# Kernel tuning notes

Hardware: AMD Instinct MI355X
Metric: run time of the kernel (lower is better)

The kernel has to match this reference:

```python
import jax, jax.numpy as jnp
import numpy as np

B, SMAX, TMAX, D = 8, 4096, 4096, 528


def setup_inputs() -> dict:
    key = jax.random.key(0)
    ks = jax.random.split(key, 20)
    src_lens = (np.arange(B) * 256 + 2048).astype(np.int64)  # 2048..3840, sum 23552
    tgt_lens = (np.arange(B) * 224 + 2304).astype(np.int64)  # 2304..3872, sum 24704
    Ns, Nt = int(src_lens.sum()), int(tgt_lens.sum())
    N = Ns + Nt  # 48256 packed coarse points (src then tgt)
    src_mask = jnp.asarray(np.arange(SMAX)[None, :] < src_lens[:, None])
    tgt_mask = jnp.asarray(np.arange(TMAX)[None, :] < tgt_lens[:, None])
    sics = np.concatenate([b * SMAX + np.arange(l) for b, l in enumerate(src_lens)])
    tics = np.concatenate([b * TMAX + np.arange(l) for b, l in enumerate(tgt_lens)])
    w = lambda k, shape: (jax.random.normal(k, shape, jnp.float32) * 0.02)
    return dict(
        geo_feats=jax.random.normal(ks[0], (N, D), jnp.float32),
        pcd=jax.random.normal(ks[1], (N, 3), jnp.float32),
        Wi1=w(ks[2], (528, 528)), bi1=w(ks[3], (528,)),
        Wi2=w(ks[4], (1024, 528)), bi2=w(ks[5], (1024,)),
        Wc1=w(ks[6], (528, 528)), bc1=w(ks[7], (528,)),
        Wc2=w(ks[8], (1024, 528)), bc2=w(ks[9], (1024,)),
        Ws1=w(ks[10], (512, 2576)), bs1=w(ks[11], (512,)),
        Ws2=w(ks[12], (256, 512)), bs2=w(ks[13], (256,)),
        Ws3=w(ks[14], (1, 256)), bs3=w(ks[15], (1,)),
        src_mask=src_mask, tgt_mask=tgt_mask,
        src_ind_coarse_split=jnp.asarray(sics, jnp.int32),
        tgt_ind_coarse_split=jnp.asarray(tics, jnp.int32),
        src_ind_coarse=jnp.arange(Ns, dtype=jnp.int32),
        tgt_ind_coarse=Ns + jnp.arange(Nt, dtype=jnp.int32),
    )


def _scatter(vals, flat_idx, b, n, d):
    # split_feats: zeros[b*n, d]; out[flat_idx] = vals; view(b, n, d)
    return jnp.zeros((b * n, d), vals.dtype).at[flat_idx].set(vals).reshape(b, n, d)


def _pw(x, W, b):
    # pointwise Conv1d(in->out, k=1) as a batched matmul over positions
    return jnp.einsum('bnd,od->bno', x, W) + b


def reference(geo_feats, pcd, Wi1, bi1, Wi2, bi2, Wc1, bc1, Wc2, bc2,
              Ws1, bs1, Ws2, bs2, Ws3, bs3,
              src_mask, tgt_mask, src_ind_coarse_split, tgt_ind_coarse_split,
              src_ind_coarse, tgt_ind_coarse):
    b, smax = src_mask.shape
    tmax = tgt_mask.shape[1]
    d = geo_feats.shape[-1]

    # split_feats: ragged gather -> padded [B, pts_max, D]
    src_feats = _scatter(geo_feats[src_ind_coarse], src_ind_coarse_split, b, smax, d)
    tgt_feats = _scatter(geo_feats[tgt_ind_coarse], tgt_ind_coarse_split, b, tmax, d)
    s_pcd = _scatter(pcd[src_ind_coarse], src_ind_coarse_split, b, smax, 3)
    t_pcd = _scatter(pcd[tgt_ind_coarse], tgt_ind_coarse_split, b, tmax, 3)

    sm = src_mask.astype(src_feats.dtype)
    tm = tgt_mask.astype(tgt_feats.dtype)

    # inst_global over valid src points (per-sample slice -> masked mean)
    h = jax.nn.relu(_pw(src_feats, Wi1, bi1))
    h = jax.nn.relu(_pw(h, Wi2, bi2))                      # [B, Smax, 1024]
    inst_g = jnp.einsum('bno,bn->bo', h, sm) / sm.sum(1, keepdims=True)

    # category_global over valid tgt points
    g = jax.nn.relu(_pw(tgt_feats, Wc1, bc1))
    g = jax.nn.relu(_pw(g, Wc2, bc2))                      # [B, Tmax, 1024]
    cat_g = jnp.einsum('bno,bn->bo', g, tm) / tm.sum(1, keepdims=True)

    # scale_net on concat(src_feats, inst_g, cat_g) without materializing [B,N,2576]:
    # split first conv weight over the concat axis; globals contribute per-batch constants
    Ws1_s, Ws1_i, Ws1_c = Ws1[:, :d], Ws1[:, d:d + 1024], Ws1[:, d + 1024:]
    glob = inst_g @ Ws1_i.T + cat_g @ Ws1_c.T + bs1        # [B, 512]
    z = jax.nn.relu(jnp.einsum('bnd,od->bno', src_feats, Ws1_s) + glob[:, None, :])
    z = jax.nn.relu(_pw(z, Ws2, bs2))                      # [B, Smax, 256]
    s = _pw(z, Ws3, bs3)                                   # [B, Smax, 1]
    scale_mat = jax.nn.sigmoid(s).transpose(0, 2, 1) - 0.5  # [B, 1, Smax]

    inv = 1.0 / jnp.sqrt(jnp.asarray(d, src_feats.dtype))
    return (src_feats * inv, tgt_feats * inv, s_pcd, t_pcd, scale_mat)
```

## Files before the change

### kernel.cpp

```cpp
#include <hip/hip_runtime.h>
#include <hip/hip_bf16.h>
#include <cstdint>
#include <cstddef>

typedef float f32x4 __attribute__((ext_vector_type(4)));
typedef __bf16 bf16x8v __attribute__((ext_vector_type(8)));

#define BM 128
#define BN 128
#define BK 32

__device__ __forceinline__ void gld16(const void* g, void* l) {
  __builtin_amdgcn_global_load_lds((const __attribute__((address_space(1))) void*)g,
                                   (__attribute__((address_space(3))) void*)l, 16, 0, 0);
}


__global__ void build_maps_kernel(const int* __restrict__ sics, int Ns,
                                  const int* __restrict__ tics, int Nt,
                                  int* __restrict__ cnt) {
  int j = blockIdx.x * 256 + threadIdx.x;
  if (j < Ns) {
    if (j == 0) { cnt[0] = 0; cnt[8] = Ns; }
    else { int b = sics[j] >> 12; if ((sics[j - 1] >> 12) != b) cnt[b] = j; }
  }
  if (j < Nt) {
    if (j == 0) { cnt[9] = 0; cnt[17] = Nt; }
    else { int b = tics[j] >> 12; if ((tics[j - 1] >> 12) != b) cnt[9 + b] = j; }
  }
}

struct PrepParams {
  const float* src[6];
  __hip_bfloat16* dst[6];
  int sld[6], rows[6], K[6], Kpad[6], rows_pad[6];
  float* zbuf; int ztotal;
};

__global__ void prep_kernel(PrepParams P) {
  int job = blockIdx.y;
  int i = blockIdx.x * 256 + threadIdx.x;
  if (job == 6) {
    if (i < P.ztotal) P.zbuf[i] = 0.f;
    return;
  }
  int kp = P.Kpad[job];
  int total = P.rows_pad[job] * kp;
  if (i >= total) return;
  int r = i / kp;
  int k = i - r * kp;
  float v = (r < P.rows[job] && k < P.K[job]) ? P.src[job][(size_t)r * P.sld[job] + k] : 0.f;
  P.dst[job][i] = __float2bfloat16(v);
}

template<int EPI>
__global__ __launch_bounds__(256, 2)
void gemm_kernel(const __hip_bfloat16* __restrict__ Aptr, int lda,
                 const __hip_bfloat16* __restrict__ Bw, int ldb,
                 const float* __restrict__ bias,
                 float* __restrict__ red_acc,
                 const float* __restrict__ globv,
                 const int* __restrict__ ridx,
                 __hip_bfloat16* __restrict__ outp, int ldo,
                 int M, int N, int Kpad, int storepad)
{
  __shared__ alignas(16) __hip_bfloat16 lA[BM * BK];
  __shared__ alignas(16) __hip_bfloat16 lB[BN * BK];
  const int tid  = threadIdx.x;
  const int lane = tid & 63;
  const int wave = tid >> 6;
  const int quad = lane >> 4;
  const int l16  = lane & 15;
  const int wr   = wave >> 1;
  const int wc   = wave & 1;
  const int m0   = blockIdx.x * BM;
  const int n0   = blockIdx.y * BN;

  const int srow = tid >> 2;
  const int skel = (tid & 3) << 3;
  const __hip_bfloat16* a0 = Aptr + (size_t)(m0 + srow) * lda + skel;
  const __hip_bfloat16* a1 = Aptr + (size_t)(m0 + 64 + srow) * lda + skel;
  const __hip_bfloat16* b0 = Bw + (size_t)(n0 + srow) * ldb + skel;
  const __hip_bfloat16* b1 = Bw + (size_t)(n0 + 64 + srow) * ldb + skel;
  __hip_bfloat16* lA0 = &lA[tid * 8];
  __hip_bfloat16* lA1 = &lA[2048 + tid * 8];
  __hip_bfloat16* lB0 = &lB[tid * 8];
  __hip_bfloat16* lB1 = &lB[2048 + tid * 8];

  f32x4 acc[4][4];
  const f32x4 zero4 = {0.f, 0.f, 0.f, 0.f};
#pragma unroll
  for (int i = 0; i < 4; ++i)
#pragma unroll
    for (int j = 0; j < 4; ++j) acc[i][j] = zero4;

  for (int k0 = 0; k0 < Kpad; k0 += BK) {
    gld16(a0 + k0, lA0);
    gld16(a1 + k0, lA1);
    gld16(b0 + k0, lB0);
    gld16(b1 + k0, lB1);
    __syncthreads();
    bf16x8v af[4], bfr[4];
#pragma unroll
    for (int i = 0; i < 4; ++i) {
      af[i]  = *(const bf16x8v*)&lA[(wr * 64 + i * 16 + l16) * BK + quad * 8];
      bfr[i] = *(const bf16x8v*)&lB[(wc * 64 + i * 16 + l16) * BK + quad * 8];
    }
#pragma unroll
    for (int mi = 0; mi < 4; ++mi)
#pragma unroll
      for (int ni = 0; ni < 4; ++ni)
        acc[mi][ni] = __builtin_amdgcn_mfma_f32_16x16x32_bf16(af[mi], bfr[ni], acc[mi][ni], 0, 0, 0);
    __syncthreads();
  }

  if (EPI == 1) {
    const int b0r = ridx[m0] >> 12;
#pragma unroll
    for (int ni = 0; ni < 4; ++ni) {
      const int col = n0 + wc * 64 + ni * 16 + l16;
      const bool colok = col < N;
      const float bcol = colok ? bias[col] : 0.f;
#pragma unroll
      for (int mi = 0; mi < 4; ++mi) {
        float v0 = 0.f, v1 = 0.f;
#pragma unroll
        for (int r = 0; r < 4; ++r) {
          const int row = m0 + wr * 64 + mi * 16 + quad * 4 + r;
          const float v = fmaxf(acc[mi][ni][r] + bcol, 0.f);
          const int b = ridx[row] >> 12;
          if (b == b0r) v0 += v; else v1 += v;
        }
        v0 += __shfl_xor(v0, 16, 64); v0 += __shfl_xor(v0, 32, 64);
        v1 += __shfl_xor(v1, 16, 64); v1 += __shfl_xor(v1, 32, 64);
        if (quad == 0 && colok) {
          atomicAdd(&red_acc[b0r * N + col], v0);
          if (b0r + 1 < 8 && v1 != 0.f) atomicAdd(&red_acc[(b0r + 1) * N + col], v1);
        }
      }
    }
  } else {
#pragma unroll
    for (int mi = 0; mi < 4; ++mi) {
#pragma unroll
      for (int r = 0; r < 4; ++r) {
        const int row = m0 + wr * 64 + mi * 16 + quad * 4 + r;
        int b = 0;
        if (EPI == 2) b = ridx[row] >> 12;
#pragma unroll
        for (int ni = 0; ni < 4; ++ni) {
          const int col = n0 + wc * 64 + ni * 16 + l16;
          if (col < N) {
            float v = acc[mi][ni][r];
            v += (EPI == 2) ? globv[b * N + col] : bias[col];
            v = fmaxf(v, 0.f);
            outp[(size_t)row * ldo + col] = __float2bfloat16(v);
          } else if (col < storepad) {
            outp[(size_t)row * ldo + col] = __float2bfloat16(0.f);
          }
        }
      }
    }
  }
}

__global__ __launch_bounds__(256) void glob_kernel(const float* __restrict__ iacc,
                                                   const float* __restrict__ cacc,
                                                   const int* __restrict__ cnt,
                                                   const float* __restrict__ Ws1,
                                                   const float* __restrict__ bs1,
                                                   float* __restrict__ globv) {
  int w    = (blockIdx.x * 256 + threadIdx.x) >> 6;
  int lane = threadIdx.x & 63;
  int b = w >> 9;
  int o = w & 511;
  const float* wi  = Ws1 + (size_t)o * 2576 + 528;
  const float* wcp = Ws1 + (size_t)o * 2576 + 1552;
  float a1 = 0.f, a2 = 0.f;
  for (int k = lane; k < 1024; k += 64) {
    a1 += iacc[b * 1024 + k] * wi[k];
    a2 += cacc[b * 1024 + k] * wcp[k];
  }
  for (int off = 32; off; off >>= 1) {
    a1 += __shfl_xor(a1, off, 64);
    a2 += __shfl_xor(a2, off, 64);
  }
  if (lane == 0) {
    float ns = (float)(cnt[b + 1] - cnt[b]);
    float nt = (float)(cnt[9 + b + 1] - cnt[9 + b]);
    globv[b * 512 + o] = bs1[o] + a1 / ns + a2 / nt;
  }
}

__global__ __launch_bounds__(256) void s_empty_kernel(const float* __restrict__ globv,
                                                      const float* __restrict__ Ws2,
                                                      const float* __restrict__ bs2,
                                                      const float* __restrict__ Ws3,
                                                      const float* __restrict__ bs3,
                                                      float* __restrict__ semp) {
  __shared__ float zrow[512];
  __shared__ float wsum[4];
  int b = blockIdx.x, t = threadIdx.x;
  zrow[t]       = fmaxf(globv[b * 512 + t], 0.f);
  zrow[t + 256] = fmaxf(globv[b * 512 + t + 256], 0.f);
  __syncthreads();
  float acc = bs2[t];
  for (int o = 0; o < 512; ++o) acc += zrow[o] * Ws2[t * 512 + o];
  float p = fmaxf(acc, 0.f) * Ws3[t];
  for (int off = 32; off; off >>= 1) p += __shfl_xor(p, off, 64);
  if ((t & 63) == 0) wsum[t >> 6] = p;
  __syncthreads();
  if (t == 0) semp[b] = wsum[0] + wsum[1] + wsum[2] + wsum[3] + bs3[0];
}

__global__ __launch_bounds__(256) void s_dot_kernel(const __hip_bfloat16* __restrict__ z2,
                                                    const float* __restrict__ Ws3,
                                                    const float* __restrict__ bs3,
                                                    float* __restrict__ sbuf, int M) {
  int w = (blockIdx.x * 256 + threadIdx.x) >> 6;
  int lane = threadIdx.x & 63;
  if (w >= M) return;
  const __hip_bfloat16* zr = z2 + (size_t)w * 256;
  float a = 0.f;
  for (int k = lane; k < 256; k += 64) a += __bfloat162float(zr[k]) * Ws3[k];
  for (int off = 32; off; off >>= 1) a += __shfl_xor(a, off, 64);
  if (lane == 0) sbuf[w] = a + bs3[0];
}

__global__ __launch_bounds__(128)
void fill_feats_kernel(const float* __restrict__ geo, const float* __restrict__ pcd,
                       const int* __restrict__ cnt,
                       float* __restrict__ out0, float* __restrict__ out1,
                       float* __restrict__ out2, float* __restrict__ out3,
                       __hip_bfloat16* __restrict__ geo_b, int Ns, float inv) {
  int bid = blockIdx.x;
  bool is_t = bid >= 32768;
  int pos = is_t ? bid - 32768 : bid;
  int b = pos >> 12, r = pos & 4095;
  int base = is_t ? cnt[9 + b] : cnt[b];
  int lim  = (is_t ? cnt[9 + b + 1] : cnt[b + 1]) - base;
  int t = threadIdx.x;
  float* op = (is_t ? out1 : out0) + (size_t)pos * 528;
  float* pp = (is_t ? out3 : out2) + (size_t)pos * 3;
  if (r < lim) {
    int src_row = (is_t ? Ns : 0) + base + r;
    const float4* g = (const float4*)(geo + (size_t)src_row * 528);
    ushort4* gb = (ushort4*)(geo_b + (size_t)src_row * 544);
    for (int d = t; d < 136; d += 128) {
      if (d < 132) {
        float4 v = g[d];
        float4 s; s.x = v.x * inv; s.y = v.y * inv; s.z = v.z * inv; s.w = v.w * inv;
        ((float4*)op)[d] = s;
        __hip_bfloat16 h0 = __float2bfloat16(v.x), h1 = __float2bfloat16(v.y);
        __hip_bfloat16 h2 = __float2bfloat16(v.z), h3 = __float2bfloat16(v.w);
        ushort4 u;
        u.x = *(unsigned short*)&h0; u.y = *(unsigned short*)&h1;
        u.z = *(unsigned short*)&h2; u.w = *(unsigned short*)&h3;
        gb[d] = u;
      } else {
        ushort4 u = {0, 0, 0, 0};
        gb[d] = u;
      }
    }
    if (t < 3) pp[t] = pcd[(size_t)src_row * 3 + t];
  } else {
    float4 z = {0.f, 0.f, 0.f, 0.f};
    for (int d = t; d < 132; d += 128) ((float4*)op)[d] = z;
    if (t < 3) pp[t] = 0.f;
  }
}

__global__ void scale_kernel(const float* __restrict__ sbuf,
                             const float* __restrict__ semp,
                             const int* __restrict__ cnt,
                             float* __restrict__ out4) {
  int i = blockIdx.x * 256 + threadIdx.x;
  if (i >= 32768) return;
  int b = i >> 12, r = i & 4095;
  int base = cnt[b];
  int lim = cnt[b + 1] - base;
  float s = (r < lim) ? sbuf[base + r] : semp[b];
  out4[i] = 1.f / (1.f + expf(-s)) - 0.5f;
}


extern "C" void kernel_launch(void* const* d_in, const int* in_sizes, int n_in,
                              void* d_out, int out_size, void* d_ws, size_t ws_size,
                              hipStream_t stream) {
  const float* geo = (const float*)d_in[0];
  const float* pcd = (const float*)d_in[1];
  const float* Wi1 = (const float*)d_in[2];
  const float* bi1 = (const float*)d_in[3];
  const float* Wi2 = (const float*)d_in[4];
  const float* bi2 = (const float*)d_in[5];
  const float* Wc1 = (const float*)d_in[6];
  const float* bc1 = (const float*)d_in[7];
  const float* Wc2 = (const float*)d_in[8];
  const float* bc2 = (const float*)d_in[9];
  const float* Ws1 = (const float*)d_in[10];
  const float* bs1 = (const float*)d_in[11];
  const float* Ws2 = (const float*)d_in[12];
  const float* bs2 = (const float*)d_in[13];
  const float* Ws3 = (const float*)d_in[14];
  const float* bs3 = (const float*)d_in[15];
  const int* sics = (const int*)d_in[18];
  const int* tics = (const int*)d_in[19];
  const int Ns = in_sizes[18];
  const int Nt = in_sizes[19];

  float* out0 = (float*)d_out;
  float* out1 = out0 + (size_t)8 * 4096 * 528;
  float* out2 = out1 + (size_t)8 * 4096 * 528;
  float* out3 = out2 + (size_t)8 * 4096 * 3;
  float* out4 = out3 + (size_t)8 * 4096 * 3;

  char* wp = (char*)d_ws;
  auto alloc = [&](size_t bytes) -> void* {
    void* p = (void*)wp;
    wp += (bytes + 255) & ~(size_t)255;
    return p;
  };
  int*   cnt   = (int*)  alloc(128);
  float* iacc  = (float*)alloc((size_t)8 * 1024 * 4);
  float* cacc  = (float*)alloc((size_t)8 * 1024 * 4);
  float* globb = (float*)alloc((size_t)8 * 512 * 4);
  float* semp  = (float*)alloc(64);
  float* sbuf  = (float*)alloc((size_t)Ns * 4);
  __hip_bfloat16* Wi1b  = (__hip_bfloat16*)alloc((size_t)640  * 544 * 2);
  __hip_bfloat16* Wi2b  = (__hip_bfloat16*)alloc((size_t)1024 * 544 * 2);
  __hip_bfloat16* Wc1b  = (__hip_bfloat16*)alloc((size_t)640  * 544 * 2);
  __hip_bfloat16* Wc2b  = (__hip_bfloat16*)alloc((size_t)1024 * 544 * 2);
  __hip_bfloat16* Ws1sb = (__hip_bfloat16*)alloc((size_t)512  * 544 * 2);
  __hip_bfloat16* Ws2b  = (__hip_bfloat16*)alloc((size_t)256  * 512 * 2);
  __hip_bfloat16* geo_b = (__hip_bfloat16*)alloc((size_t)(Ns + Nt) * 544 * 2);
  __hip_bfloat16* big   = (__hip_bfloat16*)alloc((size_t)Nt * 544 * 2);
  __hip_bfloat16* z2b   = (__hip_bfloat16*)alloc((size_t)Ns * 256 * 2);

  {
    int n = Ns > Nt ? Ns : Nt;
    build_maps_kernel<<<dim3((n + 255) / 256), dim3(256), 0, stream>>>(sics, Ns, tics, Nt, cnt);
  }
  {
    PrepParams P;
    const float* srcs[6]     = {Wi1, Wi2, Wc1, Wc2, Ws1, Ws2};
    __hip_bfloat16* dsts[6]  = {Wi1b, Wi2b, Wc1b, Wc2b, Ws1sb, Ws2b};
    int slds[6] = {528, 528, 528, 528, 2576, 512};
    int rows[6] = {528, 1024, 528, 1024, 512, 256};
    int Ks[6]   = {528, 528, 528, 528, 528, 512};
    int Kps[6]  = {544, 544, 544, 544, 544, 512};
    int rps[6]  = {640, 1024, 640, 1024, 512, 256};
    for (int i = 0; i < 6; ++i) {
      P.src[i] = srcs[i]; P.dst[i] = dsts[i]; P.sld[i] = slds[i];
      P.rows[i] = rows[i]; P.K[i] = Ks[i]; P.Kpad[i] = Kps[i]; P.rows_pad[i] = rps[i];
    }
    P.zbuf = iacc; P.ztotal = 16384;
    prep_kernel<<<dim3(2176, 7), dim3(256), 0, stream>>>(P);
  }

  float inv = 1.0f / sqrtf(528.0f);
  fill_feats_kernel<<<dim3(65536), dim3(128), 0, stream>>>(
      geo, pcd, cnt, out0, out1, out2, out3, geo_b, Ns, inv);

  gemm_kernel<0><<<dim3(Ns / 128, 5), dim3(256), 0, stream>>>(
      geo_b, 544, Wi1b, 544, bi1, nullptr, nullptr, nullptr, big, 544, Ns, 528, 544, 544);
  gemm_kernel<1><<<dim3(Ns / 128, 8), dim3(256), 0, stream>>>(
      big, 544, Wi2b, 544, bi2, iacc, nullptr, sics, nullptr, 0, Ns, 1024, 544, 0);
  gemm_kernel<0><<<dim3(Nt / 128, 5), dim3(256), 0, stream>>>(
      geo_b + (size_t)Ns * 544, 544, Wc1b, 544, bc1, nullptr, nullptr, nullptr, big, 544, Nt, 528, 544, 544);
  gemm_kernel<1><<<dim3(Nt / 128, 8), dim3(256), 0, stream>>>(
      big, 544, Wc2b, 544, bc2, cacc, nullptr, tics, nullptr, 0, Nt, 1024, 544, 0);

  glob_kernel<<<dim3(1024), dim3(256), 0, stream>>>(iacc, cacc, cnt, Ws1, bs1, globb);
  s_empty_kernel<<<dim3(8), dim3(256), 0, stream>>>(globb, Ws2, bs2, Ws3, bs3, semp);

  gemm_kernel<2><<<dim3(Ns / 128, 4), dim3(256), 0, stream>>>(
      geo_b, 544, Ws1sb, 544, nullptr, nullptr, globb, sics, big, 512, Ns, 512, 544, 512);
  gemm_kernel<0><<<dim3(Ns / 128, 2), dim3(256), 0, stream>>>(
      big, 512, Ws2b, 512, bs2, nullptr, nullptr, nullptr, z2b, 256, Ns, 256, 512, 256);

  s_dot_kernel<<<dim3((Ns + 3) / 4), dim3(256), 0, stream>>>(z2b, Ws3, bs3, sbuf, Ns);
  scale_kernel<<<dim3(128), dim3(256), 0, stream>>>(sbuf, semp, cnt, out4);
}
```

Measured before the change: 581.8 us.

## Merge GEMM launches into grouped kernels and fuse prep, fill, and dot steps

Merges the prep, map-building and geo bf16 conversion into one prep launch. Groups the three first-layer GEMMs (instance, category and scale-net first conv without the global term) into one launch, and the two 1024-wide reduction GEMMs plus the feature copy into another. The global term and ReLU are added afterwards by a fix-up kernel. The last GEMM fuses the Ws3 dot via atomics, which removes the z2 buffer and the s_dot kernel. K is padded to 576 with a BK=64 inner loop. The aim is to cut launch count and tail effects and to overlap memory-bound copies with compute, at the cost of an extra bf16 round trip on the pre-activation and float atomics.

```diff
diff --git a/kernel.cpp b/kernel.cpp
--- a/kernel.cpp
+++ b/kernel.cpp
@@ -5,10 +5,7 @@
 
 typedef float f32x4 __attribute__((ext_vector_type(4)));
 typedef __bf16 bf16x8v __attribute__((ext_vector_type(8)));
-
-#define BM 128
-#define BN 128
-#define BK 32
+typedef __hip_bfloat16 bf16;
 
 __device__ __forceinline__ void gld16(const void* g, void* l) {
   __builtin_amdgcn_global_load_lds((const __attribute__((address_space(1))) void*)g,
@@ -16,150 +13,296 @@
 }
 
 
-__global__ void build_maps_kernel(const int* __restrict__ sics, int Ns,
-                                  const int* __restrict__ tics, int Nt,
-                                  int* __restrict__ cnt) {
-  int j = blockIdx.x * 256 + threadIdx.x;
-  if (j < Ns) {
-    if (j == 0) { cnt[0] = 0; cnt[8] = Ns; }
-    else { int b = sics[j] >> 12; if ((sics[j - 1] >> 12) != b) cnt[b] = j; }
-  }
-  if (j < Nt) {
-    if (j == 0) { cnt[9] = 0; cnt[17] = Nt; }
-    else { int b = tics[j] >> 12; if ((tics[j - 1] >> 12) != b) cnt[9 + b] = j; }
-  }
-}
-
-struct PrepParams {
-  const float* src[6];
-  __hip_bfloat16* dst[6];
-  int sld[6], rows[6], K[6], Kpad[6], rows_pad[6];
+struct PrepP {
+  const float* Wsrc[6];
+  bf16* Wdst[6];
+  int sld[6], rows[6], K[6], Kpad[6];
+  int off[10];
   float* zbuf; int ztotal;
+  const float* geo; bf16* geo_b; int Nrows;
+  const int* sics; const int* tics; int Ns, Nt; int* cnt;
 };
 
-__global__ void prep_kernel(PrepParams P) {
-  int job = blockIdx.y;
-  int i = blockIdx.x * 256 + threadIdx.x;
-  if (job == 6) {
+__global__ void prep_kernel(PrepP P) {
+  int blk = blockIdx.x;
+  int job = 0;
+  while (job < 8 && blk >= P.off[job + 1]) ++job;
+  int local = blk - P.off[job];
+  if (job < 6) {
+    int i = local * 256 + threadIdx.x;
+    int kp = P.Kpad[job];
+    int total = P.rows[job] * kp;
+    if (i < total) {
+      int r = i / kp, k = i - r * kp;
+      float v = (k < P.K[job]) ? P.Wsrc[job][(size_t)r * P.sld[job] + k] : 0.f;
+      P.Wdst[job][i] = __float2bfloat16(v);
+    }
+  } else if (job == 6) {
+    int i = local * 256 + threadIdx.x;
     if (i < P.ztotal) P.zbuf[i] = 0.f;
-    return;
-  }
-  int kp = P.Kpad[job];
-  int total = P.rows_pad[job] * kp;
-  if (i >= total) return;
-  int r = i / kp;
-  int k = i - r * kp;
-  float v = (r < P.rows[job] && k < P.K[job]) ? P.src[job][(size_t)r * P.sld[job] + k] : 0.f;
-  P.dst[job][i] = __float2bfloat16(v);
-}
-
-template<int EPI>
-__global__ __launch_bounds__(256, 2)
-void gemm_kernel(const __hip_bfloat16* __restrict__ Aptr, int lda,
-                 const __hip_bfloat16* __restrict__ Bw, int ldb,
-                 const float* __restrict__ bias,
-                 float* __restrict__ red_acc,
-                 const float* __restrict__ globv,
-                 const int* __restrict__ ridx,
-                 __hip_bfloat16* __restrict__ outp, int ldo,
-                 int M, int N, int Kpad, int storepad)
+  } else if (job == 7) {
+    int t = local * 256 + threadIdx.x;
+    int row = t / 72, c8 = t - row * 72;
+    if (row < P.Nrows) {
+      int col = c8 * 8;
+      bf16* dst = P.geo_b + (size_t)row * 576 + col;
+      if (c8 < 66) {
+        const float* s = P.geo + (size_t)row * 528 + col;
+        float4 f0 = ((const float4*)s)[0], f1 = ((const float4*)s)[1];
+        bf16 h[8] = {__float2bfloat16(f0.x), __float2bfloat16(f0.y),
+                     __float2bfloat16(f0.z), __float2bfloat16(f0.w),
+                     __float2bfloat16(f1.x), __float2bfloat16(f1.y),
+                     __float2bfloat16(f1.z), __float2bfloat16(f1.w)};
+        ((uint4*)dst)[0] = *(uint4*)h;
+      } else {
+        uint4 z = {0u, 0u, 0u, 0u};
+        ((uint4*)dst)[0] = z;
+      }
+    }
+  } else {
+    int j = local * 256 + threadIdx.x;
+    if (j < P.Ns) {
+      if (j == 0) { P.cnt[0] = 0; P.cnt[8] = P.Ns; }
+      else { int b = P.sics[j] >> 12; if ((P.sics[j - 1] >> 12) != b) P.cnt[b] = j; }
+    }
+    if (j < P.Nt) {
+      if (j == 0) { P.cnt[9] = 0; P.cnt[17] = P.Nt; }
+      else { int b = P.tics[j] >> 12; if ((P.tics[j - 1] >> 12) != b) P.cnt[9 + b] = j; }
+    }
+  }
+}
+
+__device__ __forceinline__ void gemm_core(
+    const bf16* __restrict__ Aptr, int lda,
+    const bf16* __restrict__ Bw, int ldb,
+    int m0, int n0, int kiters,
+    bf16* __restrict__ lA, bf16* __restrict__ lB,
+    f32x4 acc[4][4])
 {
-  __shared__ alignas(16) __hip_bfloat16 lA[BM * BK];
-  __shared__ alignas(16) __hip_bfloat16 lB[BN * BK];
   const int tid  = threadIdx.x;
   const int lane = tid & 63;
-  const int wave = tid >> 6;
   const int quad = lane >> 4;
   const int l16  = lane & 15;
-  const int wr   = wave >> 1;
-  const int wc   = wave & 1;
-  const int m0   = blockIdx.x * BM;
-  const int n0   = blockIdx.y * BN;
-
+  const int wr   = tid >> 7;
+  const int wc   = (tid >> 6) & 1;
   const int srow = tid >> 2;
-  const int skel = (tid & 3) << 3;
-  const __hip_bfloat16* a0 = Aptr + (size_t)(m0 + srow) * lda + skel;
-  const __hip_bfloat16* a1 = Aptr + (size_t)(m0 + 64 + srow) * lda + skel;
-  const __hip_bfloat16* b0 = Bw + (size_t)(n0 + srow) * ldb + skel;
-  const __hip_bfloat16* b1 = Bw + (size_t)(n0 + 64 + srow) * ldb + skel;
-  __hip_bfloat16* lA0 = &lA[tid * 8];
-  __hip_bfloat16* lA1 = &lA[2048 + tid * 8];
-  __hip_bfloat16* lB0 = &lB[tid * 8];
-  __hip_bfloat16* lB1 = &lB[2048 + tid * 8];
+  const int scol = (tid & 3) << 3;
+  const bf16* aA0 = Aptr + (size_t)(m0 + srow) * lda + scol;
+  const bf16* aA1 = aA0 + (size_t)64 * lda;
+  const bf16* aB0 = Bw + (size_t)(n0 + srow) * ldb + scol;
+  const bf16* aB1 = aB0 + (size_t)64 * ldb;
+  bf16* lA00 = lA + tid * 8;        bf16* lA01 = lA + 2048 + tid * 8;
+  bf16* lA10 = lA + 4096 + tid * 8; bf16* lA11 = lA + 6144 + tid * 8;
+  bf16* lB00 = lB + tid * 8;        bf16* lB01 = lB + 2048 + tid * 8;
+  bf16* lB10 = lB + 4096 + tid * 8; bf16* lB11 = lB + 6144 + tid * 8;
+
+  for (int k = 0; k < kiters; ++k) {
+    const int k0 = k * 64;
+    gld16(aA0 + k0, lA00);      gld16(aA1 + k0, lA01);
+    gld16(aA0 + k0 + 32, lA10); gld16(aA1 + k0 + 32, lA11);
+    gld16(aB0 + k0, lB00);      gld16(aB1 + k0, lB01);
+    gld16(aB0 + k0 + 32, lB10); gld16(aB1 + k0 + 32, lB11);
+    __syncthreads();
+#pragma unroll
+    for (int kk = 0; kk < 2; ++kk) {
+      bf16x8v af[4], bfr[4];
+#pragma unroll
+      for (int i = 0; i < 4; ++i) {
+        af[i]  = *(const bf16x8v*)&lA[kk * 4096 + (wr * 64 + i * 16 + l16) * 32 + quad * 8];
+        bfr[i] = *(const bf16x8v*)&lB[kk * 4096 + (wc * 64 + i * 16 + l16) * 32 + quad * 8];
+      }
+#pragma unroll
+      for (int mi = 0; mi < 4; ++mi)
+#pragma unroll
+        for (int ni = 0; ni < 4; ++ni)
+          acc[mi][ni] = __builtin_amdgcn_mfma_f32_16x16x32_bf16(af[mi], bfr[ni], acc[mi][ni], 0, 0, 0);
+    }
+    __syncthreads();
+  }
+}
+
+__global__ __launch_bounds__(256, 2)
+void kernelA(const bf16* __restrict__ geo_b,
+             const bf16* __restrict__ Wi1b, const bf16* __restrict__ Wc1b,
+             const bf16* __restrict__ Ws1sb,
+             const float* __restrict__ bi1, const float* __restrict__ bc1,
+             bf16* __restrict__ big_s, bf16* __restrict__ big_t,
+             bf16* __restrict__ zpre, int Ms, int Mt)
+{
+  __shared__ alignas(16) bf16 lA[8192], lB[8192];
+  const int x = blockIdx.x;
+  const int e0 = Ms * 5, e1 = e0 + Mt * 5;
+  const bf16 *A, *B; const float* bias = nullptr; bf16* out;
+  int m0, n0, ldo, epi;
+  if (x < e0) {
+    int mt = x / 5, nt = x - mt * 5;
+    m0 = mt * 128; n0 = nt * 128;
+    A = geo_b; B = Wi1b; bias = bi1; out = big_s; ldo = 576; epi = 0;
+  } else if (x < e1) {
+    int y = x - e0; int mt = y / 5, nt = y - mt * 5;
+    m0 = mt * 128; n0 = nt * 128;
+    A = geo_b + (size_t)Ms * 128 * 576; B = Wc1b; bias = bc1; out = big_t; ldo = 576; epi = 0;
+  } else {
+    int y = x - e1; int mt = y / 4, nt = y - mt * 4;
+    m0 = mt * 128; n0 = nt * 128;
+    A = geo_b; B = Ws1sb; out = zpre; ldo = 512; epi = 1;
+  }
 
   f32x4 acc[4][4];
-  const f32x4 zero4 = {0.f, 0.f, 0.f, 0.f};
+  const f32x4 z4 = {0.f, 0.f, 0.f, 0.f};
 #pragma unroll
   for (int i = 0; i < 4; ++i)
 #pragma unroll
-    for (int j = 0; j < 4; ++j) acc[i][j] = zero4;
-
-  for (int k0 = 0; k0 < Kpad; k0 += BK) {
-    gld16(a0 + k0, lA0);
-    gld16(a1 + k0, lA1);
-    gld16(b0 + k0, lB0);
-    gld16(b1 + k0, lB1);
-    __syncthreads();
-    bf16x8v af[4], bfr[4];
-#pragma unroll
-    for (int i = 0; i < 4; ++i) {
-      af[i]  = *(const bf16x8v*)&lA[(wr * 64 + i * 16 + l16) * BK + quad * 8];
-      bfr[i] = *(const bf16x8v*)&lB[(wc * 64 + i * 16 + l16) * BK + quad * 8];
-    }
-#pragma unroll
-    for (int mi = 0; mi < 4; ++mi)
-#pragma unroll
-      for (int ni = 0; ni < 4; ++ni)
-        acc[mi][ni] = __builtin_amdgcn_mfma_f32_16x16x32_bf16(af[mi], bfr[ni], acc[mi][ni], 0, 0, 0);
-    __syncthreads();
-  }
-
-  if (EPI == 1) {
-    const int b0r = ridx[m0] >> 12;
-#pragma unroll
-    for (int ni = 0; ni < 4; ++ni) {
-      const int col = n0 + wc * 64 + ni * 16 + l16;
-      const bool colok = col < N;
-      const float bcol = colok ? bias[col] : 0.f;
-#pragma unroll
-      for (int mi = 0; mi < 4; ++mi) {
-        float v0 = 0.f, v1 = 0.f;
-#pragma unroll
-        for (int r = 0; r < 4; ++r) {
-          const int row = m0 + wr * 64 + mi * 16 + quad * 4 + r;
-          const float v = fmaxf(acc[mi][ni][r] + bcol, 0.f);
-          const int b = ridx[row] >> 12;
-          if (b == b0r) v0 += v; else v1 += v;
+    for (int j = 0; j < 4; ++j) acc[i][j] = z4;
+
+  gemm_core(A, 576, B, 576, m0, n0, 9, lA, lB, acc);
+
+  const int lane = threadIdx.x & 63, quad = lane >> 4, l16 = lane & 15;
+  const int wr = threadIdx.x >> 7, wc = (threadIdx.x >> 6) & 1;
+#pragma unroll
+  for (int mi = 0; mi < 4; ++mi) {
+#pragma unroll
+    for (int r = 0; r < 4; ++r) {
+      const int row = m0 + wr * 64 + mi * 16 + quad * 4 + r;
+#pragma unroll
+      for (int ni = 0; ni < 4; ++ni) {
+        const int col = n0 + wc * 64 + ni * 16 + l16;
+        if (epi == 0) {
+          if (col < 528)
+            out[(size_t)row * ldo + col] = __float2bfloat16(fmaxf(acc[mi][ni][r] + bias[col], 0.f));
+          else if (col < 576)
+            out[(size_t)row * ldo + col] = __float2bfloat16(0.f);
+        } else {
+          out[(size_t)row * ldo + col] = __float2bfloat16(acc[mi][ni][r]);
         }
-        v0 += __shfl_xor(v0, 16, 64); v0 += __shfl_xor(v0, 32, 64);
-        v1 += __shfl_xor(v1, 16, 64); v1 += __shfl_xor(v1, 32, 64);
-        if (quad == 0 && colok) {
-          atomicAdd(&red_acc[b0r * N + col], v0);
-          if (b0r + 1 < 8 && v1 != 0.f) atomicAdd(&red_acc[(b0r + 1) * N + col], v1);
-        }
-      }
-    }
+      }
+    }
+  }
+}
+
+__global__ __launch_bounds__(256, 2)
+void kernelB(const bf16* __restrict__ big_s, const bf16* __restrict__ big_t,
+             const bf16* __restrict__ Wi2b, const bf16* __restrict__ Wc2b,
+             const float* __restrict__ bi2, const float* __restrict__ bc2,
+             float* __restrict__ iacc, float* __restrict__ cacc,
+             const int* __restrict__ sics, const int* __restrict__ tics,
+             int Ms, int Mt,
+             const float* __restrict__ geo, const float* __restrict__ pcd,
+             const int* __restrict__ cnt,
+             float* __restrict__ out0, float* __restrict__ out1,
+             float* __restrict__ out2, float* __restrict__ out3,
+             int Ns, float inv)
+{
+  __shared__ alignas(16) bf16 lA[8192], lB[8192];
+  const int x = blockIdx.x;
+  const int e0 = Ms * 8, e1 = e0 + Mt * 8;
+  if (x >= e1) {
+    int f = x - e1;
+    int lane = threadIdx.x & 63;
+    int rv = f * 4 + (threadIdx.x >> 6);
+    bool is_t = rv >= 32768;
+    int pos = is_t ? rv - 32768 : rv;
+    int b = pos >> 12, r = pos & 4095;
+    int base = is_t ? cnt[9 + b] : cnt[b];
+    int lim  = (is_t ? cnt[9 + b + 1] : cnt[b + 1]) - base;
+    float* op = (is_t ? out1 : out0) + (size_t)pos * 528;
+    float* pp = (is_t ? out3 : out2) + (size_t)pos * 3;
+    if (r < lim) {
+      int sr = (is_t ? Ns : 0) + base + r;
+      const float4* g = (const float4*)(geo + (size_t)sr * 528);
+      for (int d = lane; d < 132; d += 64) {
+        float4 v = g[d];
+        float4 s = {v.x * inv, v.y * inv, v.z * inv, v.w * inv};
+        ((float4*)op)[d] = s;
+      }
+      if (lane < 3) pp[lane] = pcd[(size_t)sr * 3 + lane];
+    } else {
+      float4 z = {0.f, 0.f, 0.f, 0.f};
+      for (int d = lane; d < 132; d += 64) ((float4*)op)[d] = z;
+      if (lane < 3) pp[lane] = 0.f;
+    }
+    return;
+  }
+  const bf16 *A, *B; const float* bias; float* red; const int* ridx;
+  int m0, n0;
+  if (x < e0) {
+    int mt = x / 8, nt = x - mt * 8;
+    m0 = mt * 128; n0 = nt * 128;
+    A = big_s; B = Wi2b; bias = bi2; red = iacc; ridx = sics;
   } else {
+    int y = x - e0; int mt = y / 8, nt = y - mt * 8;
+    m0 = mt * 128; n0 = nt * 128;
+    A = big_t; B = Wc2b; bias = bc2; red = cacc; ridx = tics;
+  }
+
+  f32x4 acc[4][4];
+  const f32x4 z4 = {0.f, 0.f, 0.f, 0.f};
+#pragma unroll
+  for (int i = 0; i < 4; ++i)
+#pragma unroll
+    for (int j = 0; j < 4; ++j) acc[i][j] = z4;
+
+  gemm_core(A, 576, B, 576, m0, n0, 9, lA, lB, acc);
+
+  const int lane = threadIdx.x & 63, quad = lane >> 4, l16 = lane & 15;
+  const int wr = threadIdx.x >> 7, wc = (threadIdx.x >> 6) & 1;
+  const int b0r = ridx[m0] >> 12;
+#pragma unroll
+  for (int ni = 0; ni < 4; ++ni) {
+    const int col = n0 + wc * 64 + ni * 16 + l16;
+    const float bcol = bias[col];
 #pragma unroll
     for (int mi = 0; mi < 4; ++mi) {
+      float v0 = 0.f, v1 = 0.f;
 #pragma unroll
       for (int r = 0; r < 4; ++r) {
         const int row = m0 + wr * 64 + mi * 16 + quad * 4 + r;
-        int b = 0;
-        if (EPI == 2) b = ridx[row] >> 12;
-#pragma unroll
-        for (int ni = 0; ni < 4; ++ni) {
-          const int col = n0 + wc * 64 + ni * 16 + l16;
-          if (col < N) {
-            float v = acc[mi][ni][r];
-            v += (EPI == 2) ? globv[b * N + col] : bias[col];
-            v = fmaxf(v, 0.f);
-            outp[(size_t)row * ldo + col] = __float2bfloat16(v);
-          } else if (col < storepad) {
-            outp[(size_t)row * ldo + col] = __float2bfloat16(0.f);
-          }
-        }
-      }
+        const float v = fmaxf(acc[mi][ni][r] + bcol, 0.f);
+        const int b = ridx[row] >> 12;
+        if (b == b0r) v0 += v; else v1 += v;
+      }
+      v0 += __shfl_xor(v0, 16, 64); v0 += __shfl_xor(v0, 32, 64);
+      v1 += __shfl_xor(v1, 16, 64); v1 += __shfl_xor(v1, 32, 64);
+      if (quad == 0) {
+        atomicAdd(&red[b0r * 1024 + col], v0);
+        if (b0r + 1 < 8 && v1 != 0.f) atomicAdd(&red[(b0r + 1) * 1024 + col], v1);
+      }
+    }
+  }
+}
+
+__global__ __launch_bounds__(256, 2)
+void kernelC(const bf16* __restrict__ zpre, const bf16* __restrict__ Ws2b,
+             const float* __restrict__ bs2, const float* __restrict__ Ws3,
+             float* __restrict__ sbuf)
+{
+  __shared__ alignas(16) bf16 lA[8192], lB[8192];
+  const int m0 = blockIdx.x * 128, n0 = blockIdx.y * 128;
+  f32x4 acc[4][4];
+  const f32x4 z4 = {0.f, 0.f, 0.f, 0.f};
+#pragma unroll
+  for (int i = 0; i < 4; ++i)
+#pragma unroll
+    for (int j = 0; j < 4; ++j) acc[i][j] = z4;
+
+  gemm_core(zpre, 512, Ws2b, 512, m0, n0, 8, lA, lB, acc);
+
+  const int lane = threadIdx.x & 63, quad = lane >> 4, l16 = lane & 15;
+  const int wr = threadIdx.x >> 7, wc = (threadIdx.x >> 6) & 1;
+#pragma unroll
+  for (int mi = 0; mi < 4; ++mi) {
+#pragma unroll
+    for (int r = 0; r < 4; ++r) {
+      const int row = m0 + wr * 64 + mi * 16 + quad * 4 + r;
+      float p = 0.f;
+#pragma unroll
+      for (int ni = 0; ni < 4; ++ni) {
+        const int col = n0 + wc * 64 + ni * 16 + l16;
+        p += fmaxf(acc[mi][ni][r] + bs2[col], 0.f) * Ws3[col];
+      }
+      p += __shfl_xor(p, 1, 64); p += __shfl_xor(p, 2, 64);
+      p += __shfl_xor(p, 4, 64); p += __shfl_xor(p, 8, 64);
+      if (l16 == 0) atomicAdd(&sbuf[row], p);
     }
   }
 }
@@ -213,73 +356,33 @@
   if (t == 0) semp[b] = wsum[0] + wsum[1] + wsum[2] + wsum[3] + bs3[0];
 }
 
-__global__ __launch_bounds__(256) void s_dot_kernel(const __hip_bfloat16* __restrict__ z2,
-                                                    const float* __restrict__ Ws3,
-                                                    const float* __restrict__ bs3,
-                                                    float* __restrict__ sbuf, int M) {
-  int w = (blockIdx.x * 256 + threadIdx.x) >> 6;
-  int lane = threadIdx.x & 63;
-  if (w >= M) return;
-  const __hip_bfloat16* zr = z2 + (size_t)w * 256;
-  float a = 0.f;
-  for (int k = lane; k < 256; k += 64) a += __bfloat162float(zr[k]) * Ws3[k];
-  for (int off = 32; off; off >>= 1) a += __shfl_xor(a, off, 64);
-  if (lane == 0) sbuf[w] = a + bs3[0];
-}
-
-__global__ __launch_bounds__(128)
-void fill_feats_kernel(const float* __restrict__ geo, const float* __restrict__ pcd,
-                       const int* __restrict__ cnt,
-                       float* __restrict__ out0, float* __restrict__ out1,
-                       float* __restrict__ out2, float* __restrict__ out3,
-                       __hip_bfloat16* __restrict__ geo_b, int Ns, float inv) {
-  int bid = blockIdx.x;
-  bool is_t = bid >= 32768;
-  int pos = is_t ? bid - 32768 : bid;
-  int b = pos >> 12, r = pos & 4095;
-  int base = is_t ? cnt[9 + b] : cnt[b];
-  int lim  = (is_t ? cnt[9 + b + 1] : cnt[b + 1]) - base;
-  int t = threadIdx.x;
-  float* op = (is_t ? out1 : out0) + (size_t)pos * 528;
-  float* pp = (is_t ? out3 : out2) + (size_t)pos * 3;
-  if (r < lim) {
-    int src_row = (is_t ? Ns : 0) + base + r;
-    const float4* g = (const float4*)(geo + (size_t)src_row * 528);
-    ushort4* gb = (ushort4*)(geo_b + (size_t)src_row * 544);
-    for (int d = t; d < 136; d += 128) {
-      if (d < 132) {
-        float4 v = g[d];
-        float4 s; s.x = v.x * inv; s.y = v.y * inv; s.z = v.z * inv; s.w = v.w * inv;
-        ((float4*)op)[d] = s;
-        __hip_bfloat16 h0 = __float2bfloat16(v.x), h1 = __float2bfloat16(v.y);
-        __hip_bfloat16 h2 = __float2bfloat16(v.z), h3 = __float2bfloat16(v.w);
-        ushort4 u;
-        u.x = *(unsigned short*)&h0; u.y = *(unsigned short*)&h1;
-        u.z = *(unsigned short*)&h2; u.w = *(unsigned short*)&h3;
-        gb[d] = u;
-      } else {
-        ushort4 u = {0, 0, 0, 0};
-        gb[d] = u;
-      }
-    }
-    if (t < 3) pp[t] = pcd[(size_t)src_row * 3 + t];
-  } else {
-    float4 z = {0.f, 0.f, 0.f, 0.f};
-    for (int d = t; d < 132; d += 128) ((float4*)op)[d] = z;
-    if (t < 3) pp[t] = 0.f;
-  }
+__global__ void zfix_kernel(bf16* __restrict__ z, const float* __restrict__ globv,
+                            const int* __restrict__ sics, int total) {
+  int idx = blockIdx.x * 256 + threadIdx.x;
+  if (idx >= total) return;
+  int row = idx >> 6, c0 = (idx & 63) << 3;
+  int b = sics[row] >> 12;
+  const float* gv = globv + b * 512 + c0;
+  bf16* zp = z + (size_t)row * 512 + c0;
+  uint4 u = *(uint4*)zp;
+  bf16* e = (bf16*)&u;
+#pragma unroll
+  for (int i = 0; i < 8; ++i)
+    e[i] = __float2bfloat16(fmaxf(__bfloat162float(e[i]) + gv[i], 0.f));
+  *(uint4*)zp = u;
 }
 
 __global__ void scale_kernel(const float* __restrict__ sbuf,
                              const float* __restrict__ semp,
                              const int* __restrict__ cnt,
+                             const float* __restrict__ bs3,
                              float* __restrict__ out4) {
   int i = blockIdx.x * 256 + threadIdx.x;
   if (i >= 32768) return;
   int b = i >> 12, r = i & 4095;
   int base = cnt[b];
   int lim = cnt[b + 1] - base;
-  float s = (r < lim) ? sbuf[base + r] : semp[b];
+  float s = (r < lim) ? sbuf[base + r] + bs3[0] : semp[b];
   out4[i] = 1.f / (1.f + expf(-s)) - 0.5f;
 }
 
@@ -307,6 +410,8 @@
   const int* tics = (const int*)d_in[19];
   const int Ns = in_sizes[18];
   const int Nt = in_sizes[19];
+  const int Ms = Ns / 128, Mt = Nt / 128;
+  const int Nrows = Ns + Nt;
 
   float* out0 = (float*)d_out;
   float* out1 = out0 + (size_t)8 * 4096 * 528;
@@ -323,61 +428,60 @@
   int*   cnt   = (int*)  alloc(128);
   float* iacc  = (float*)alloc((size_t)8 * 1024 * 4);
   float* cacc  = (float*)alloc((size_t)8 * 1024 * 4);
+  float* sbuf  = (float*)alloc((size_t)Ns * 4);
   float* globb = (float*)alloc((size_t)8 * 512 * 4);
   float* semp  = (float*)alloc(64);
-  float* sbuf  = (float*)alloc((size_t)Ns * 4);
-  __hip_bfloat16* Wi1b  = (__hip_bfloat16*)alloc((size_t)640  * 544 * 2);
-  __hip_bfloat16* Wi2b  = (__hip_bfloat16*)alloc((size_t)1024 * 544 * 2);
-  __hip_bfloat16* Wc1b  = (__hip_bfloat16*)alloc((size_t)640  * 544 * 2);
-  __hip_bfloat16* Wc2b  = (__hip_bfloat16*)alloc((size_t)1024 * 544 * 2);
-  __hip_bfloat16* Ws1sb = (__hip_bfloat16*)alloc((size_t)512  * 544 * 2);
-  __hip_bfloat16* Ws2b  = (__hip_bfloat16*)alloc((size_t)256  * 512 * 2);
-  __hip_bfloat16* geo_b = (__hip_bfloat16*)alloc((size_t)(Ns + Nt) * 544 * 2);
-  __hip_bfloat16* big   = (__hip_bfloat16*)alloc((size_t)Nt * 544 * 2);
-  __hip_bfloat16* z2b   = (__hip_bfloat16*)alloc((size_t)Ns * 256 * 2);
-
+  bf16* Wi1b  = (bf16*)alloc((size_t)640  * 576 * 2);
+  bf16* Wi2b  = (bf16*)alloc((size_t)1024 * 576 * 2);
+  bf16* Wc1b  = (bf16*)alloc((size_t)640  * 576 * 2);
+  bf16* Wc2b  = (bf16*)alloc((size_t)1024 * 576 * 2);
+  bf16* Ws1sb = (bf16*)alloc((size_t)512  * 576 * 2);
+  bf16* Ws2b  = (bf16*)alloc((size_t)256  * 512 * 2);
+  bf16* geo_b = (bf16*)alloc((size_t)Nrows * 576 * 2);
+  bf16* big_s = (bf16*)alloc((size_t)Ns * 576 * 2);
+  bf16* big_t = (bf16*)alloc((size_t)Nt * 576 * 2);
+  bf16* zpre  = (bf16*)alloc((size_t)Ns * 512 * 2);
+
+  PrepP P;
   {
-    int n = Ns > Nt ? Ns : Nt;
-    build_maps_kernel<<<dim3((n + 255) / 256), dim3(256), 0, stream>>>(sics, Ns, tics, Nt, cnt);
-  }
-  {
-    PrepParams P;
-    const float* srcs[6]     = {Wi1, Wi2, Wc1, Wc2, Ws1, Ws2};
-    __hip_bfloat16* dsts[6]  = {Wi1b, Wi2b, Wc1b, Wc2b, Ws1sb, Ws2b};
+    const float* srcs[6] = {Wi1, Wi2, Wc1, Wc2, Ws1, Ws2};
+    bf16* dsts[6]        = {Wi1b, Wi2b, Wc1b, Wc2b, Ws1sb, Ws2b};
     int slds[6] = {528, 528, 528, 528, 2576, 512};
     int rows[6] = {528, 1024, 528, 1024, 512, 256};
     int Ks[6]   = {528, 528, 528, 528, 528, 512};
-    int Kps[6]  = {544, 544, 544, 544, 544, 512};
-    int rps[6]  = {640, 1024, 640, 1024, 512, 256};
+    int Kps[6]  = {576, 576, 576, 576, 576, 512};
+    int nblk = 0;
     for (int i = 0; i < 6; ++i) {
-      P.src[i] = srcs[i]; P.dst[i] = dsts[i]; P.sld[i] = slds[i];
-      P.rows[i] = rows[i]; P.K[i] = Ks[i]; P.Kpad[i] = Kps[i]; P.rows_pad[i] = rps[i];
-    }
-    P.zbuf = iacc; P.ztotal = 16384;
-    prep_kernel<<<dim3(2176, 7), dim3(256), 0, stream>>>(P);
-  }
+      P.Wsrc[i] = srcs[i]; P.Wdst[i] = dsts[i]; P.sld[i] = slds[i];
+      P.rows[i] = rows[i]; P.K[i] = Ks[i]; P.Kpad[i] = Kps[i];
+      P.off[i] = nblk;
+      nblk += (rows[i] * Kps[i] + 255) / 256;
+    }
+    P.off[6] = nblk;
+    P.zbuf = iacc; P.ztotal = 8192 + 8192 + Ns;
+    nblk += (P.ztotal + 255) / 256;
+    P.off[7] = nblk;
+    P.geo = geo; P.geo_b = geo_b; P.Nrows = Nrows;
+    nblk += ((Nrows * 72) + 255) / 256;
+    P.off[8] = nblk;
+    P.sics = sics; P.tics = tics; P.Ns = Ns; P.Nt = Nt; P.cnt = cnt;
+    int n = Ns > Nt ? Ns : Nt;
+    nblk += (n + 255) / 256;
+    P.off[9] = nblk;
+    prep_kernel<<<dim3(nblk), dim3(256), 0, stream>>>(P);
+  }
+
+  kernelA<<<dim3(Ms * 5 + Mt * 5 + Ms * 4), dim3(256), 0, stream>>>(
+      geo_b, Wi1b, Wc1b, Ws1sb, bi1, bc1, big_s, big_t, zpre, Ms, Mt);
 
   float inv = 1.0f / sqrtf(528.0f);
-  fill_feats_kernel<<<dim3(65536), dim3(128), 0, stream>>>(
-      geo, pcd, cnt, out0, out1, out2, out3, geo_b, Ns, inv);
-
-  gemm_kernel<0><<<dim3(Ns / 128, 5), dim3(256), 0, stream>>>(
-      geo_b, 544, Wi1b, 544, bi1, nullptr, nullptr, nullptr, big, 544, Ns, 528, 544, 544);
-  gemm_kernel<1><<<dim3(Ns / 128, 8), dim3(256), 0, stream>>>(
-      big, 544, Wi2b, 544, bi2, iacc, nullptr, sics, nullptr, 0, Ns, 1024, 544, 0);
-  gemm_kernel<0><<<dim3(Nt / 128, 5), dim3(256), 0, stream>>>(
-      geo_b + (size_t)Ns * 544, 544, Wc1b, 544, bc1, nullptr, nullptr, nullptr, big, 544, Nt, 528, 544, 544);
-  gemm_kernel<1><<<dim3(Nt / 128, 8), dim3(256), 0, stream>>>(
-      big, 544, Wc2b, 544, bc2, cacc, nullptr, tics, nullptr, 0, Nt, 1024, 544, 0);
+  kernelB<<<dim3(Ms * 8 + Mt * 8 + 16384), dim3(256), 0, stream>>>(
+      big_s, big_t, Wi2b, Wc2b, bi2, bc2, iacc, cacc, sics, tics, Ms, Mt,
+      geo, pcd, cnt, out0, out1, out2, out3, Ns, inv);
 
   glob_kernel<<<dim3(1024), dim3(256), 0, stream>>>(iacc, cacc, cnt, Ws1, bs1, globb);
   s_empty_kernel<<<dim3(8), dim3(256), 0, stream>>>(globb, Ws2, bs2, Ws3, bs3, semp);
-
-  gemm_kernel<2><<<dim3(Ns / 128, 4), dim3(256), 0, stream>>>(
-      geo_b, 544, Ws1sb, 544, nullptr, nullptr, globb, sics, big, 512, Ns, 512, 544, 512);
-  gemm_kernel<0><<<dim3(Ns / 128, 2), dim3(256), 0, stream>>>(
-      big, 512, Ws2b, 512, bs2, nullptr, nullptr, nullptr, z2b, 256, Ns, 256, 512, 256);
-
-  s_dot_kernel<<<dim3((Ns + 3) / 4), dim3(256), 0, stream>>>(z2b, Ws3, bs3, sbuf, Ns);
-  scale_kernel<<<dim3(128), dim3(256), 0, stream>>>(sbuf, semp, cnt, out4);
-}
+  zfix_kernel<<<dim3((Ns * 64 + 255) / 256), dim3(256), 0, stream>>>(zpre, globb, sics, Ns * 64);
+  kernelC<<<dim3(Ms, 2), dim3(256), 0, stream>>>(zpre, Ws2b, bs2, Ws3, sbuf);
+  scale_kernel<<<dim3(128), dim3(256), 0, stream>>>(sbuf, semp, cnt, bs3, out4);
+}
```

Result: faster. 517.0 us (-11.1%).
